# Kernel optimization log

Hardware: AMD Instinct MI355X
Metric: run time of the kernel (lower is better)

The kernel has to match this reference:

```python
import jax, jax.numpy as jnp
import numpy as np

NUM_HEADS = 16


def setup_inputs() -> dict:
    key = jax.random.key(0)
    k1, k2, k3 = jax.random.split(key, 3)
    B, N, C = 2, 2048, 1024
    x = jax.random.normal(k1, (B, N, C), dtype=jnp.float32)
    w_qkv = jax.random.normal(k2, (3 * C, C), dtype=jnp.float32) * (C ** -0.5)
    w_proj = jax.random.normal(k3, (C, C), dtype=jnp.float32) * (C ** -0.5)
    b_proj = jnp.zeros((C,), dtype=jnp.float32)
    return {"x": x, "w_qkv": w_qkv, "w_proj": w_proj, "b_proj": b_proj}


def reference(x, w_qkv, w_proj, b_proj):
    B, N, C = x.shape
    H = NUM_HEADS
    D = C // H
    scale = 1.0 / jnp.sqrt(jnp.asarray(D, x.dtype))
    qkv = (x @ w_qkv.T).reshape(B, N, 3, H, D)
    qkv = jnp.transpose(qkv, (2, 0, 3, 1, 4))  # [3,B,H,N,D]
    q, k, v = qkv[0], qkv[1], qkv[2]
    # scaled dot-product attention with explicit score matrix [B,H,N,N]
    attn = jnp.einsum('bhnd,bhmd->bhnm', q, k) * scale
    attn = jax.nn.softmax(attn, axis=-1)
    out = jnp.einsum('bhnm,bhmd->bhnd', attn, v)
    out = jnp.transpose(out, (0, 2, 1, 3)).reshape(B, N, C)
    # output projection
    return out @ w_proj.T + b_proj
```

## Files before the change

kernel.cpp:

```cpp
#include <hip/hip_runtime.h>

typedef unsigned short u16;
typedef __attribute__((ext_vector_type(8))) short bf16x8;
typedef __attribute__((ext_vector_type(4))) float f32x4;
typedef __attribute__((ext_vector_type(16))) float f32x16;
typedef __attribute__((ext_vector_type(4))) unsigned u32x4;

#define B_ 2
#define N_ 2048
#define C_ 1024
#define H_ 16
#define D_ 64
#define M_ (B_ * N_)

#define QSCALE 0.18033688011114336f

#define EXP2R(x) __builtin_amdgcn_exp2f(x)

__device__ __forceinline__ u16 f2bf(float f) {
    union { float f; unsigned u; } x; x.f = f;
    return (u16)((x.u + 0x8000u) >> 16);
}
__device__ __forceinline__ unsigned pack2bf(float a, float b) {
    union { float f; unsigned u; } x, y; x.f = a; y.f = b;
    return __builtin_amdgcn_perm(y.u + 0x8000u, x.u + 0x8000u, 0x07060302);
}
__device__ __forceinline__ unsigned cvtpk2bf(float a, float b) {
    unsigned r;
    asm("v_cvt_pk_bf16_f32 %0, %1, %2" : "=v"(r) : "v"(a), "v"(b));
    return r;
}

__device__ __forceinline__ void async_copy16(const void* gsrc, void* ldst) {
    __builtin_amdgcn_global_load_lds(
        (__attribute__((address_space(1))) void*)gsrc,
        (__attribute__((address_space(3))) void*)ldst,
        16, 0, 0);
}

__global__ void cast3_kernel(const float* __restrict__ x, const float* __restrict__ wq,
                             const float* __restrict__ wp, u16* __restrict__ xo,
                             u16* __restrict__ wqo, u16* __restrict__ wpo) {
    int b = blockIdx.x;
    const float* s; u16* d;
    if (b < 4096)      { s = x;  d = xo;  }
    else if (b < 7168) { s = wq; d = wqo; b -= 4096; }
    else               { s = wp; d = wpo; b -= 7168; }
    int i = (b * 256 + threadIdx.x) * 4;
    const float4 v = *(const float4*)(s + i);
    uint2 o;
    o.x = pack2bf(v.x, v.y);
    o.y = pack2bf(v.z, v.w);
    *(uint2*)(d + i) = o;
}

__global__ __launch_bounds__(512, 2) void gemm_qkv8(
    const u16* __restrict__ A, const u16* __restrict__ Bm,
    u16* __restrict__ qo, u16* __restrict__ ko, u16* __restrict__ vt) {
    __shared__ u16 L[2][4][8192];
    const int tid = threadIdx.x, lane = tid & 63, w = tid >> 6;
    const int wm = w >> 2, wn = w & 3;
    const int q16 = lane >> 4, l15 = lane & 15, l7 = lane & 7;
    const int lr3 = lane >> 3, lc7 = lane & 7;
    const int sbid = (blockIdx.x & 7) * 24 + (blockIdx.x >> 3);
    const int bx = sbid % 12, by = sbid / 12;
    const int m0 = by * 256, n0 = bx * 256;
    const int cswz8 = (lc7 ^ lr3) * 8;

    auto stageHT = [&](int t, int isB, int h) {
        if (t > 15) return;
        const u16* src = isB ? Bm : A;
        int base_row = (isB ? n0 : m0) + h * 128;
#pragma unroll
        for (int i = 0; i < 2; ++i) {
            int c = w * 2 + i;
            async_copy16(src + (size_t)(base_row + c * 8 + lr3) * 1024 + t * 64 + cswz8,
                         (char*)L + ((t & 1) * 4 + isB * 2 + h) * 16384 + c * 1024);
        }
    };

    stageHT(0, 0, 0); stageHT(0, 1, 0); stageHT(0, 1, 1); stageHT(0, 0, 1);
    stageHT(1, 0, 0); stageHT(1, 1, 0); stageHT(1, 1, 1);
    asm volatile("s_waitcnt vmcnt(6)" ::: "memory");
    __builtin_amdgcn_s_barrier();

    f32x4 acc[8][4] = {};
    const int aRow = l15 * 64;
    const int colsw0 = (q16 ^ l7) * 8, colsw1 = ((4 + q16) ^ l7) * 8;
    const u16* LA[2] = { &L[0][wm][0], &L[1][wm][0] };
    const u16* LB[2] = { &L[0][2 + (wn >> 1)][0], &L[1][2 + (wn >> 1)][0] };
    const int bOff = (wn & 1) * 4096;

    bf16x8 Af[4][2], Bf0[2][2], Bf1[2][2];

    auto readA = [&](int P, int mh) {
#pragma unroll
        for (int i = 0; i < 4; ++i) {
            Af[i][0] = *(const bf16x8*)(LA[P] + (mh * 64 + i * 16) * 64 + aRow + colsw0);
            Af[i][1] = *(const bf16x8*)(LA[P] + (mh * 64 + i * 16) * 64 + aRow + colsw1);
        }
    };
    auto readB = [&](int P, int nh, bf16x8 (*Bf)[2]) {
#pragma unroll
        for (int j = 0; j < 2; ++j) {
            Bf[j][0] = *(const bf16x8*)(LB[P] + bOff + (nh * 32 + j * 16) * 64 + aRow + colsw0);
            Bf[j][1] = *(const bf16x8*)(LB[P] + bOff + (nh * 32 + j * 16) * 64 + aRow + colsw1);
        }
    };
    auto mfma16 = [&](int mh, int nh, bf16x8 (*Bf)[2]) {
        __builtin_amdgcn_s_setprio(1);
#pragma unroll
        for (int i = 0; i < 4; ++i)
#pragma unroll
            for (int j = 0; j < 2; ++j)
#pragma unroll
                for (int ks = 0; ks < 2; ++ks)
                    acc[mh * 4 + i][nh * 2 + j] = __builtin_amdgcn_mfma_f32_16x16x32_bf16(
                        Af[i][ks], Bf[j][ks], acc[mh * 4 + i][nh * 2 + j], 0, 0, 0);
        __builtin_amdgcn_s_setprio(0);
    };

    for (int it = 0; it < 8; ++it) {
        const int T = 2 * it;
        readA(0, 0); readB(0, 0, Bf0); stageHT(T + 1, 0, 1);
        __builtin_amdgcn_s_barrier();
        mfma16(0, 0, Bf0);
        __builtin_amdgcn_s_barrier();
        readB(0, 1, Bf1);
        __builtin_amdgcn_s_barrier();
        mfma16(0, 1, Bf1);
        __builtin_amdgcn_s_barrier();
        readA(0, 1); stageHT(T + 2, 1, 0);
        __builtin_amdgcn_s_barrier();
        mfma16(1, 1, Bf1);
        __builtin_amdgcn_s_barrier();
        stageHT(T + 2, 1, 1); stageHT(T + 2, 0, 0);
        __builtin_amdgcn_s_barrier();
        mfma16(1, 0, Bf0);
        if (it < 7) { asm volatile("s_waitcnt vmcnt(6)" ::: "memory"); }
        else        { asm volatile("s_waitcnt vmcnt(0)" ::: "memory"); }
        __builtin_amdgcn_s_barrier();
        readA(1, 0); readB(1, 0, Bf0); stageHT(T + 2, 0, 1);
        __builtin_amdgcn_s_barrier();
        mfma16(0, 0, Bf0);
        __builtin_amdgcn_s_barrier();
        readB(1, 1, Bf1);
        __builtin_amdgcn_s_barrier();
        mfma16(0, 1, Bf1);
        __builtin_amdgcn_s_barrier();
        readA(1, 1); stageHT(T + 3, 1, 0);
        __builtin_amdgcn_s_barrier();
        mfma16(1, 1, Bf1);
        __builtin_amdgcn_s_barrier();
        stageHT(T + 3, 1, 1); stageHT(T + 3, 0, 0);
        __builtin_amdgcn_s_barrier();
        mfma16(1, 0, Bf0);
        if (it < 7) { asm volatile("s_waitcnt vmcnt(6)" ::: "memory"); }
        __builtin_amdgcn_s_barrier();
    }

#pragma unroll
    for (int fm = 0; fm < 8; ++fm) {
#pragma unroll
        for (int fn = 0; fn < 4; ++fn) {
            int n_g = n0 + wn * 64 + fn * 16 + l15;
            int which = n_g >> 10;
            int h = (n_g >> 6) & 15;
            int d = n_g & 63;
            int m_base = m0 + wm * 128 + fm * 16 + q16 * 4;
            int b = m_base >> 11;
            int nn0 = m_base & 2047;
            if (which == 2) {
                uint2 pk;
                pk.x = pack2bf(acc[fm][fn][0], acc[fm][fn][1]);
                pk.y = pack2bf(acc[fm][fn][2], acc[fm][fn][3]);
                *(uint2*)(vt + ((size_t)((b * H_ + h) * D_ + d) << 11) + nn0) = pk;
            } else {
                size_t base = ((size_t)((b * H_ + h) * N_ + nn0) << 6) + d;
#pragma unroll
                for (int r = 0; r < 4; ++r) {
                    float v = acc[fm][fn][r];
                    if (which == 0) qo[base + (size_t)r * D_] = f2bf(v * QSCALE);
                    else            ko[base + (size_t)r * D_] = f2bf(v);
                }
            }
        }
    }
}

__global__ __launch_bounds__(256, 2) void gemm_out(
    const u16* __restrict__ A, const u16* __restrict__ Bm,
    const float* __restrict__ bias, float* __restrict__ out) {
    __shared__ u16 As[128 * 64];
    __shared__ u16 Bs[64 * 64];
    const int K = C_, Ncols = C_, ntiles_n = 16;
    const int tid = threadIdx.x, lane = tid & 63, w = tid >> 6;
    const int cpx = gridDim.x >> 3;
    const int sbid = (blockIdx.x & 7) * cpx + (blockIdx.x >> 3);
    const int bx = sbid % ntiles_n, by = sbid / ntiles_n;
    const int m0 = by * 128, n0 = bx * 64;
    const int wm = w >> 1, wn = w & 1;
    const int q16 = lane >> 4, l15 = lane & 15;
    const int r0 = lane >> 3, c0 = (lane & 7) * 8;
    f32x4 acc[4][2] = {};

    for (int k0 = 0; k0 < K; k0 += 64) {
#pragma unroll
        for (int i = 0; i < 4; ++i) {
            int blk = w * 4 + i;
            int r = blk * 8 + r0;
            async_copy16(A + (size_t)(m0 + r) * K + k0 + c0, (char*)As + blk * 1024);
        }
#pragma unroll
        for (int i = 0; i < 2; ++i) {
            int blk = w * 2 + i;
            int r = blk * 8 + r0;
            async_copy16(Bm + (size_t)(n0 + r) * K + k0 + c0, (char*)Bs + blk * 1024);
        }
        __builtin_amdgcn_s_waitcnt(0);
        __syncthreads();
#pragma unroll
        for (int ks = 0; ks < 2; ++ks) {
            bf16x8 af[4], bf[2];
#pragma unroll
            for (int i = 0; i < 4; ++i)
                af[i] = *(const bf16x8*)&As[(wm * 64 + i * 16 + l15) * 64 + ks * 32 + q16 * 8];
#pragma unroll
            for (int i = 0; i < 2; ++i)
                bf[i] = *(const bf16x8*)&Bs[(wn * 32 + i * 16 + l15) * 64 + ks * 32 + q16 * 8];
#pragma unroll
            for (int mi = 0; mi < 4; ++mi)
#pragma unroll
                for (int ni = 0; ni < 2; ++ni)
                    acc[mi][ni] = __builtin_amdgcn_mfma_f32_16x16x32_bf16(af[mi], bf[ni], acc[mi][ni], 0, 0, 0);
        }
        __syncthreads();
    }

#pragma unroll
    for (int mi = 0; mi < 4; ++mi) {
#pragma unroll
        for (int ni = 0; ni < 2; ++ni) {
            int n_g = n0 + wn * 32 + ni * 16 + l15;
#pragma unroll
            for (int r = 0; r < 4; ++r) {
                int m_g = m0 + wm * 64 + mi * 16 + q16 * 4 + r;
                out[(size_t)m_g * Ncols + n_g] = acc[mi][ni][r] + bias[n_g];
            }
        }
    }
}

__global__ __launch_bounds__(512, 1) void attn_kernel(
    const u16* __restrict__ Q, const u16* __restrict__ K,
    const u16* __restrict__ VT, u16* __restrict__ O) {
    __shared__ u16 Ks[2][2][64 * 64];
    __shared__ u16 Vs[2][2][64 * 64];
    const int tid = threadIdx.x, lane = tid & 63, w = tid >> 6;
    const int l31 = lane & 31, hi = lane >> 5, l7 = l31 & 7;
    const int bid = blockIdx.x;
    const int bh = (bid & 7) * 4 + (bid >> 6);
    const int q0 = ((bid >> 3) & 7) * 256;
    const size_t head = (size_t)bh * N_ * D_;
    const int lr3 = lane >> 3, lc7 = lane & 7;

    auto stage = [&](int kt, int buf) {
        int key0 = kt * 128;
        int row = w * 8 + lr3;
#pragma unroll
        for (int s = 0; s < 2; ++s) {
            async_copy16(K + head + (size_t)(key0 + s * 64 + row) * D_ + (lc7 ^ lr3) * 8,
                         (char*)Ks[buf][s] + w * 1024);
            async_copy16(VT + head + (size_t)row * N_ + key0 + s * 64 + (lc7 ^ lr3) * 8,
                         (char*)Vs[buf][s] + w * 1024);
        }
    };

    bf16x8 qf[4];
#pragma unroll
    for (int ds = 0; ds < 4; ++ds)
        qf[ds] = *(const bf16x8*)(Q + head + (size_t)(q0 + w * 32 + l31) * D_ + ds * 16 + hi * 8);
    stage(0, 0);
    __builtin_amdgcn_s_waitcnt(0);
    __syncthreads();

    f32x16 o_acc[2] = {};
    float rs = 0.f;

    for (int kt = 0; kt < 16; ++kt) {
        int buf = kt & 1;
        stage((kt + 1) & 15, buf ^ 1);

#pragma unroll
        for (int s = 0; s < 2; ++s) {
#pragma unroll
            for (int kb2 = 0; kb2 < 2; ++kb2) {
                f32x16 st = {};
                __builtin_amdgcn_s_setprio(1);
#pragma unroll
                for (int ds = 0; ds < 4; ++ds) {
                    bf16x8 kf = *(const bf16x8*)&Ks[buf][s][(kb2 * 32 + l31) * 64 + ((ds * 2 + hi) ^ l7) * 8];
                    st = __builtin_amdgcn_mfma_f32_32x32x16_bf16(kf, qf[ds], st, 0, 0, 0);
                }
                __builtin_amdgcn_s_setprio(0);

                float p[16];
#pragma unroll
                for (int i = 0; i < 16; ++i) p[i] = EXP2R(st[i]);
#pragma unroll
                for (int i = 0; i < 16; ++i) rs += p[i];

                unsigned a0 = cvtpk2bf(p[0], p[1]),   b0 = cvtpk2bf(p[4], p[5]);
                unsigned a1 = cvtpk2bf(p[2], p[3]),   b1 = cvtpk2bf(p[6], p[7]);
                unsigned a2 = cvtpk2bf(p[8], p[9]),   b2 = cvtpk2bf(p[12], p[13]);
                unsigned a3 = cvtpk2bf(p[10], p[11]), b3 = cvtpk2bf(p[14], p[15]);
                asm("v_permlane32_swap_b32 %0, %1" : "+v"(a0), "+v"(b0));
                asm("v_permlane32_swap_b32 %0, %1" : "+v"(a1), "+v"(b1));
                asm("v_permlane32_swap_b32 %0, %1" : "+v"(a2), "+v"(b2));
                asm("v_permlane32_swap_b32 %0, %1" : "+v"(a3), "+v"(b3));
                union { u32x4 u; bf16x8 v; } af0, af1;
                af0.u = (u32x4){a0, a1, b0, b1};
                af1.u = (u32x4){a2, a3, b2, b3};

                __builtin_amdgcn_s_setprio(1);
#pragma unroll
                for (int db = 0; db < 2; ++db) {
                    bf16x8 vf0 = *(const bf16x8*)&Vs[buf][s][(db * 32 + l31) * 64 + ((kb2 * 4 + hi) ^ l7) * 8];
                    o_acc[db] = __builtin_amdgcn_mfma_f32_32x32x16_bf16(af0.v, vf0, o_acc[db], 0, 0, 0);
                    bf16x8 vf1 = *(const bf16x8*)&Vs[buf][s][(db * 32 + l31) * 64 + ((kb2 * 4 + 2 + hi) ^ l7) * 8];
                    o_acc[db] = __builtin_amdgcn_mfma_f32_32x32x16_bf16(af1.v, vf1, o_acc[db], 0, 0, 0);
                }
                __builtin_amdgcn_s_setprio(0);
            }
        }

        __builtin_amdgcn_s_waitcnt(0);
        __syncthreads();
    }

    rs += __shfl_xor(rs, 32);
    float rsi = 1.0f / rs;

    const int b = bh >> 4, h = bh & 15;
#pragma unroll
    for (int reg = 0; reg < 16; ++reg) {
        int qrow = (reg & 3) + 8 * (reg >> 2) + 4 * hi;
        float inv = __shfl(rsi, qrow);
        int qg = q0 + w * 32 + qrow;
#pragma unroll
        for (int db = 0; db < 2; ++db) {
            int d = db * 32 + l31;
            O[((size_t)(b * N_ + qg) << 10) + h * 64 + d] = f2bf(o_acc[db][reg] * inv);
        }
    }
}

extern "C" void kernel_launch(void* const* d_in, const int* in_sizes, int n_in,
                              void* d_out, int out_size, void* d_ws, size_t ws_size,
                              hipStream_t stream) {
    const float* x      = (const float*)d_in[0];
    const float* w_qkv  = (const float*)d_in[1];
    const float* w_proj = (const float*)d_in[2];
    const float* b_proj = (const float*)d_in[3];
    float* out = (float*)d_out;

    char* ws = (char*)d_ws;
    const size_t MB = 1024 * 1024;
    u16* x_bf     = (u16*)(ws + 0 * MB);
    u16* wqkv_bf  = (u16*)(ws + 8 * MB);
    u16* wproj_bf = (u16*)(ws + 14 * MB);
    u16* q_bf     = (u16*)(ws + 16 * MB);
    u16* k_bf     = (u16*)(ws + 24 * MB);
    u16* vt_bf    = (u16*)(ws + 32 * MB);
    u16* ao_bf    = (u16*)(ws + 40 * MB);

    cast3_kernel<<<8192, 256, 0, stream>>>(x, w_qkv, w_proj, x_bf, wqkv_bf, wproj_bf);

    gemm_qkv8<<<192, 512, 0, stream>>>(x_bf, wqkv_bf, q_bf, k_bf, vt_bf);

    attn_kernel<<<256, 512, 0, stream>>>(q_bf, k_bf, vt_bf, ao_bf);

    gemm_out<<<512, 256, 0, stream>>>(ao_bf, wproj_bf, b_proj, out);
}
```

Baseline: 175.4 us.

## Fuse cast, QKV GEMM, attention and output GEMM into persistent mega-kernel

```diff
diff --git a/kernel.cpp b/kernel.cpp
--- a/kernel.cpp
+++ b/kernel.cpp
@@ -36,6 +36,342 @@
         (__attribute__((address_space(1))) void*)gsrc,
         (__attribute__((address_space(3))) void*)ldst,
         16, 0, 0);
+}
+
+__device__ __forceinline__ void gbar(unsigned* bar) {
+    __syncthreads();
+    __threadfence();
+    if (threadIdx.x == 0) {
+        unsigned g = __hip_atomic_load(bar + 1, __ATOMIC_ACQUIRE, __HIP_MEMORY_SCOPE_AGENT);
+        unsigned old = __hip_atomic_fetch_add(bar, 1, __ATOMIC_ACQ_REL, __HIP_MEMORY_SCOPE_AGENT);
+        if (old == 255) {
+            __hip_atomic_store(bar, 0, __ATOMIC_RELAXED, __HIP_MEMORY_SCOPE_AGENT);
+            __hip_atomic_fetch_add(bar + 1, 1, __ATOMIC_ACQ_REL, __HIP_MEMORY_SCOPE_AGENT);
+        } else {
+            while (__hip_atomic_load(bar + 1, __ATOMIC_ACQUIRE, __HIP_MEMORY_SCOPE_AGENT) == g)
+                __builtin_amdgcn_s_sleep(2);
+        }
+    }
+    __syncthreads();
+}
+
+__global__ __launch_bounds__(512, 1) void mega_kernel(
+    const float* __restrict__ x, const float* __restrict__ wq,
+    const float* __restrict__ wp, const float* __restrict__ bias,
+    u16* __restrict__ x_bf, u16* __restrict__ wqkv_bf, u16* __restrict__ wproj_bf,
+    u16* __restrict__ q_bf, u16* __restrict__ k_bf, u16* __restrict__ vt_bf,
+    u16* __restrict__ ao_bf, float* __restrict__ out, unsigned* bar) {
+    __shared__ __align__(16) u16 SL[65536];
+    const int tid = threadIdx.x, bid = blockIdx.x;
+    const int lane = tid & 63, w = tid >> 6;
+
+    for (int i4 = bid * 512 + tid; i4 < 2097152; i4 += 256 * 512) {
+        const float* s; u16* d; int j = i4;
+        if (j < 1048576)      { s = x;  d = x_bf; }
+        else if (j < 1835008) { s = wq; d = wqkv_bf; j -= 1048576; }
+        else                  { s = wp; d = wproj_bf; j -= 1835008; }
+        const float4 v = *(const float4*)(s + (size_t)j * 4);
+        uint2 o;
+        o.x = pack2bf(v.x, v.y);
+        o.y = pack2bf(v.z, v.w);
+        *(uint2*)(d + (size_t)j * 4) = o;
+    }
+    gbar(bar);
+
+    if (bid < 192) {
+        u16* L = SL;
+        const int wm = w >> 2, wn = w & 3;
+        const int q16 = lane >> 4, l15 = lane & 15, l7 = lane & 7;
+        const int lr3 = lane >> 3, lc7 = lane & 7;
+        const int sbid = (bid & 7) * 24 + (bid >> 3);
+        const int bx = sbid % 12, by = sbid / 12;
+        const int m0 = by * 256, n0 = bx * 256;
+        const int cswz8 = (lc7 ^ lr3) * 8;
+
+        auto stageHT = [&](int t, int isB, int h) {
+            if (t > 15) return;
+            const u16* src = isB ? wqkv_bf : x_bf;
+            int base_row = (isB ? n0 : m0) + h * 128;
+#pragma unroll
+            for (int i = 0; i < 2; ++i) {
+                int c = w * 2 + i;
+                async_copy16(src + (size_t)(base_row + c * 8 + lr3) * 1024 + t * 64 + cswz8,
+                             (char*)L + ((t & 1) * 4 + isB * 2 + h) * 16384 + c * 1024);
+            }
+        };
+
+        stageHT(0, 0, 0); stageHT(0, 1, 0); stageHT(0, 1, 1); stageHT(0, 0, 1);
+        stageHT(1, 0, 0); stageHT(1, 1, 0); stageHT(1, 1, 1);
+        asm volatile("s_waitcnt vmcnt(6)" ::: "memory");
+        __builtin_amdgcn_s_barrier();
+
+        f32x4 acc[8][4] = {};
+        const int aRow = l15 * 64;
+        const int colsw0 = (q16 ^ l7) * 8, colsw1 = ((4 + q16) ^ l7) * 8;
+        const u16* LA[2] = { L + (0 * 4 + wm) * 8192, L + (1 * 4 + wm) * 8192 };
+        const u16* LB[2] = { L + (0 * 4 + 2 + (wn >> 1)) * 8192, L + (1 * 4 + 2 + (wn >> 1)) * 8192 };
+        const int bOff = (wn & 1) * 4096;
+
+        bf16x8 Af[4][2], Bf0[2][2], Bf1[2][2];
+
+        auto readA = [&](int P, int mh) {
+#pragma unroll
+            for (int i = 0; i < 4; ++i) {
+                Af[i][0] = *(const bf16x8*)(LA[P] + (mh * 64 + i * 16) * 64 + aRow + colsw0);
+                Af[i][1] = *(const bf16x8*)(LA[P] + (mh * 64 + i * 16) * 64 + aRow + colsw1);
+            }
+        };
+        auto readB = [&](int P, int nh, bf16x8 (*Bf)[2]) {
+#pragma unroll
+            for (int j = 0; j < 2; ++j) {
+                Bf[j][0] = *(const bf16x8*)(LB[P] + bOff + (nh * 32 + j * 16) * 64 + aRow + colsw0);
+                Bf[j][1] = *(const bf16x8*)(LB[P] + bOff + (nh * 32 + j * 16) * 64 + aRow + colsw1);
+            }
+        };
+        auto mfma16 = [&](int mh, int nh, bf16x8 (*Bf)[2]) {
+            __builtin_amdgcn_s_setprio(1);
+#pragma unroll
+            for (int i = 0; i < 4; ++i)
+#pragma unroll
+                for (int j = 0; j < 2; ++j)
+#pragma unroll
+                    for (int ks = 0; ks < 2; ++ks)
+                        acc[mh * 4 + i][nh * 2 + j] = __builtin_amdgcn_mfma_f32_16x16x32_bf16(
+                            Af[i][ks], Bf[j][ks], acc[mh * 4 + i][nh * 2 + j], 0, 0, 0);
+            __builtin_amdgcn_s_setprio(0);
+        };
+
+        for (int it = 0; it < 8; ++it) {
+            const int T = 2 * it;
+            readA(0, 0); readB(0, 0, Bf0); stageHT(T + 1, 0, 1);
+            __builtin_amdgcn_s_barrier();
+            mfma16(0, 0, Bf0);
+            __builtin_amdgcn_s_barrier();
+            readB(0, 1, Bf1);
+            __builtin_amdgcn_s_barrier();
+            mfma16(0, 1, Bf1);
+            __builtin_amdgcn_s_barrier();
+            readA(0, 1); stageHT(T + 2, 1, 0);
+            __builtin_amdgcn_s_barrier();
+            mfma16(1, 1, Bf1);
+            __builtin_amdgcn_s_barrier();
+            stageHT(T + 2, 1, 1); stageHT(T + 2, 0, 0);
+            __builtin_amdgcn_s_barrier();
+            mfma16(1, 0, Bf0);
+            if (it < 7) { asm volatile("s_waitcnt vmcnt(6)" ::: "memory"); }
+            else        { asm volatile("s_waitcnt vmcnt(0)" ::: "memory"); }
+            __builtin_amdgcn_s_barrier();
+            readA(1, 0); readB(1, 0, Bf0); stageHT(T + 2, 0, 1);
+            __builtin_amdgcn_s_barrier();
+            mfma16(0, 0, Bf0);
+            __builtin_amdgcn_s_barrier();
+            readB(1, 1, Bf1);
+            __builtin_amdgcn_s_barrier();
+            mfma16(0, 1, Bf1);
+            __builtin_amdgcn_s_barrier();
+            readA(1, 1); stageHT(T + 3, 1, 0);
+            __builtin_amdgcn_s_barrier();
+            mfma16(1, 1, Bf1);
+            __builtin_amdgcn_s_barrier();
+            stageHT(T + 3, 1, 1); stageHT(T + 3, 0, 0);
+            __builtin_amdgcn_s_barrier();
+            mfma16(1, 0, Bf0);
+            if (it < 7) { asm volatile("s_waitcnt vmcnt(6)" ::: "memory"); }
+            __builtin_amdgcn_s_barrier();
+        }
+
+#pragma unroll
+        for (int fm = 0; fm < 8; ++fm) {
+#pragma unroll
+            for (int fn = 0; fn < 4; ++fn) {
+                int n_g = n0 + wn * 64 + fn * 16 + l15;
+                int which = n_g >> 10;
+                int h = (n_g >> 6) & 15;
+                int d = n_g & 63;
+                int m_base = m0 + wm * 128 + fm * 16 + q16 * 4;
+                int b = m_base >> 11;
+                int nn0 = m_base & 2047;
+                if (which == 2) {
+                    uint2 pk;
+                    pk.x = pack2bf(acc[fm][fn][0], acc[fm][fn][1]);
+                    pk.y = pack2bf(acc[fm][fn][2], acc[fm][fn][3]);
+                    *(uint2*)(vt_bf + ((size_t)((b * H_ + h) * D_ + d) << 11) + nn0) = pk;
+                } else {
+                    size_t base = ((size_t)((b * H_ + h) * N_ + nn0) << 6) + d;
+#pragma unroll
+                    for (int r = 0; r < 4; ++r) {
+                        float v = acc[fm][fn][r];
+                        if (which == 0) q_bf[base + (size_t)r * D_] = f2bf(v * QSCALE);
+                        else            k_bf[base + (size_t)r * D_] = f2bf(v);
+                    }
+                }
+            }
+        }
+    }
+    gbar(bar);
+
+    {
+        u16* KsB = SL;
+        u16* VsB = SL + 16384;
+        const int l31 = lane & 31, hi = lane >> 5, l7 = l31 & 7;
+        const int bh = (bid & 7) * 4 + (bid >> 6);
+        const int q0 = ((bid >> 3) & 7) * 256;
+        const size_t head = (size_t)bh * N_ * D_;
+        const int lr3 = lane >> 3, lc7 = lane & 7;
+
+        auto stage = [&](int kt, int buf) {
+            int key0 = kt * 128;
+            int row = w * 8 + lr3;
+#pragma unroll
+            for (int s = 0; s < 2; ++s) {
+                async_copy16(k_bf + head + (size_t)(key0 + s * 64 + row) * D_ + (lc7 ^ lr3) * 8,
+                             (char*)(KsB + (buf * 2 + s) * 4096) + w * 1024);
+                async_copy16(vt_bf + head + (size_t)row * N_ + key0 + s * 64 + (lc7 ^ lr3) * 8,
+                             (char*)(VsB + (buf * 2 + s) * 4096) + w * 1024);
+            }
+        };
+
+        bf16x8 qf[4];
+#pragma unroll
+        for (int ds = 0; ds < 4; ++ds)
+            qf[ds] = *(const bf16x8*)(q_bf + head + (size_t)(q0 + w * 32 + l31) * D_ + ds * 16 + hi * 8);
+        stage(0, 0);
+        __builtin_amdgcn_s_waitcnt(0);
+        __syncthreads();
+
+        f32x16 o_acc[2] = {};
+        float rs = 0.f;
+
+        for (int kt = 0; kt < 16; ++kt) {
+            int buf = kt & 1;
+            stage((kt + 1) & 15, buf ^ 1);
+
+#pragma unroll
+            for (int s = 0; s < 2; ++s) {
+                const u16* Kp = KsB + (buf * 2 + s) * 4096;
+                const u16* Vp = VsB + (buf * 2 + s) * 4096;
+#pragma unroll
+                for (int kb2 = 0; kb2 < 2; ++kb2) {
+                    f32x16 st = {};
+                    __builtin_amdgcn_s_setprio(1);
+#pragma unroll
+                    for (int ds = 0; ds < 4; ++ds) {
+                        bf16x8 kf = *(const bf16x8*)(Kp + (kb2 * 32 + l31) * 64 + ((ds * 2 + hi) ^ l7) * 8);
+                        st = __builtin_amdgcn_mfma_f32_32x32x16_bf16(kf, qf[ds], st, 0, 0, 0);
+                    }
+                    __builtin_amdgcn_s_setprio(0);
+
+                    float p[16];
+#pragma unroll
+                    for (int i = 0; i < 16; ++i) p[i] = EXP2R(st[i]);
+#pragma unroll
+                    for (int i = 0; i < 16; ++i) rs += p[i];
+
+                    unsigned a0 = cvtpk2bf(p[0], p[1]),   b0 = cvtpk2bf(p[4], p[5]);
+                    unsigned a1 = cvtpk2bf(p[2], p[3]),   b1 = cvtpk2bf(p[6], p[7]);
+                    unsigned a2 = cvtpk2bf(p[8], p[9]),   b2 = cvtpk2bf(p[12], p[13]);
+                    unsigned a3 = cvtpk2bf(p[10], p[11]), b3 = cvtpk2bf(p[14], p[15]);
+                    asm("v_permlane32_swap_b32 %0, %1" : "+v"(a0), "+v"(b0));
+                    asm("v_permlane32_swap_b32 %0, %1" : "+v"(a1), "+v"(b1));
+                    asm("v_permlane32_swap_b32 %0, %1" : "+v"(a2), "+v"(b2));
+                    asm("v_permlane32_swap_b32 %0, %1" : "+v"(a3), "+v"(b3));
+                    union { u32x4 u; bf16x8 v; } af0, af1;
+                    af0.u = (u32x4){a0, a1, b0, b1};
+                    af1.u = (u32x4){a2, a3, b2, b3};
+
+                    __builtin_amdgcn_s_setprio(1);
+#pragma unroll
+                    for (int db = 0; db < 2; ++db) {
+                        bf16x8 vf0 = *(const bf16x8*)(Vp + (db * 32 + l31) * 64 + ((kb2 * 4 + hi) ^ l7) * 8);
+                        o_acc[db] = __builtin_amdgcn_mfma_f32_32x32x16_bf16(af0.v, vf0, o_acc[db], 0, 0, 0);
+                        bf16x8 vf1 = *(const bf16x8*)(Vp + (db * 32 + l31) * 64 + ((kb2 * 4 + 2 + hi) ^ l7) * 8);
+                        o_acc[db] = __builtin_amdgcn_mfma_f32_32x32x16_bf16(af1.v, vf1, o_acc[db], 0, 0, 0);
+                    }
+                    __builtin_amdgcn_s_setprio(0);
+                }
+            }
+
+            __builtin_amdgcn_s_waitcnt(0);
+            __syncthreads();
+        }
+
+        rs += __shfl_xor(rs, 32);
+        float rsi = 1.0f / rs;
+        const int b = bh >> 4, h = bh & 15;
+#pragma unroll
+        for (int reg = 0; reg < 16; ++reg) {
+            int qrow = (reg & 3) + 8 * (reg >> 2) + 4 * hi;
+            float inv = __shfl(rsi, qrow);
+            int qg = q0 + w * 32 + qrow;
+#pragma unroll
+            for (int db = 0; db < 2; ++db) {
+                int d = db * 32 + l31;
+                ao_bf[((size_t)(b * N_ + qg) << 10) + h * 64 + d] = f2bf(o_acc[db][reg] * inv);
+            }
+        }
+    }
+    gbar(bar);
+
+    {
+        const int grp = w >> 2, wv = w & 2 ? (w & 3) : (w & 3);
+        const int wv3 = w & 3;
+        u16* As = SL + grp * 12288;
+        u16* Bs = SL + grp * 12288 + 8192;
+        const int v = bid * 2 + grp;
+        const int sbid = (v & 7) * 64 + (v >> 3);
+        const int bx = sbid & 15, by = sbid >> 4;
+        const int m0 = by * 128, n0 = bx * 64;
+        const int wm = wv3 >> 1, wn = wv3 & 1;
+        const int q16 = lane >> 4, l15 = lane & 15;
+        const int r0 = lane >> 3, c0 = (lane & 7) * 8;
+        f32x4 acc[4][2] = {};
+
+        for (int k0 = 0; k0 < C_; k0 += 64) {
+#pragma unroll
+            for (int i = 0; i < 4; ++i) {
+                int blk = wv3 * 4 + i;
+                int r = blk * 8 + r0;
+                async_copy16(ao_bf + (size_t)(m0 + r) * C_ + k0 + c0, (char*)As + blk * 1024);
+            }
+#pragma unroll
+            for (int i = 0; i < 2; ++i) {
+                int blk = wv3 * 2 + i;
+                int r = blk * 8 + r0;
+                async_copy16(wproj_bf + (size_t)(n0 + r) * C_ + k0 + c0, (char*)Bs + blk * 1024);
+            }
+            __builtin_amdgcn_s_waitcnt(0);
+            __syncthreads();
+#pragma unroll
+            for (int ks = 0; ks < 2; ++ks) {
+                bf16x8 af[4], bf[2];
+#pragma unroll
+                for (int i = 0; i < 4; ++i)
+                    af[i] = *(const bf16x8*)(As + (wm * 64 + i * 16 + l15) * 64 + ks * 32 + q16 * 8);
+#pragma unroll
+                for (int i = 0; i < 2; ++i)
+                    bf[i] = *(const bf16x8*)(Bs + (wn * 32 + i * 16 + l15) * 64 + ks * 32 + q16 * 8);
+#pragma unroll
+                for (int mi = 0; mi < 4; ++mi)
+#pragma unroll
+                    for (int ni = 0; ni < 2; ++ni)
+                        acc[mi][ni] = __builtin_amdgcn_mfma_f32_16x16x32_bf16(af[mi], bf[ni], acc[mi][ni], 0, 0, 0);
+            }
+            __syncthreads();
+        }
+
+#pragma unroll
+        for (int mi = 0; mi < 4; ++mi) {
+#pragma unroll
+            for (int ni = 0; ni < 2; ++ni) {
+                int n_g = n0 + wn * 32 + ni * 16 + l15;
+#pragma unroll
+                for (int r = 0; r < 4; ++r) {
+                    int m_g = m0 + wm * 64 + mi * 16 + q16 * 4 + r;
+                    out[(size_t)m_g * C_ + n_g] = acc[mi][ni][r] + bias[n_g];
+                }
+            }
+        }
+    }
 }
 
 __global__ void cast3_kernel(const float* __restrict__ x, const float* __restrict__ wq,
@@ -54,132 +390,70 @@
     *(uint2*)(d + i) = o;
 }
 
-__global__ __launch_bounds__(512, 2) void gemm_qkv8(
+__global__ __launch_bounds__(256, 3) void gemm_qkv(
     const u16* __restrict__ A, const u16* __restrict__ Bm,
     u16* __restrict__ qo, u16* __restrict__ ko, u16* __restrict__ vt) {
-    __shared__ u16 L[2][4][8192];
+    __shared__ u16 As[128 * 64];
+    __shared__ u16 Bs[128 * 64];
+    const int K = C_, ntiles_n = 24;
     const int tid = threadIdx.x, lane = tid & 63, w = tid >> 6;
-    const int wm = w >> 2, wn = w & 3;
-    const int q16 = lane >> 4, l15 = lane & 15, l7 = lane & 7;
-    const int lr3 = lane >> 3, lc7 = lane & 7;
-    const int sbid = (blockIdx.x & 7) * 24 + (blockIdx.x >> 3);
-    const int bx = sbid % 12, by = sbid / 12;
-    const int m0 = by * 256, n0 = bx * 256;
-    const int cswz8 = (lc7 ^ lr3) * 8;
-
-    auto stageHT = [&](int t, int isB, int h) {
-        if (t > 15) return;
-        const u16* src = isB ? Bm : A;
-        int base_row = (isB ? n0 : m0) + h * 128;
-#pragma unroll
-        for (int i = 0; i < 2; ++i) {
-            int c = w * 2 + i;
-            async_copy16(src + (size_t)(base_row + c * 8 + lr3) * 1024 + t * 64 + cswz8,
-                         (char*)L + ((t & 1) * 4 + isB * 2 + h) * 16384 + c * 1024);
-        }
-    };
-
-    stageHT(0, 0, 0); stageHT(0, 1, 0); stageHT(0, 1, 1); stageHT(0, 0, 1);
-    stageHT(1, 0, 0); stageHT(1, 1, 0); stageHT(1, 1, 1);
-    asm volatile("s_waitcnt vmcnt(6)" ::: "memory");
-    __builtin_amdgcn_s_barrier();
-
-    f32x4 acc[8][4] = {};
-    const int aRow = l15 * 64;
-    const int colsw0 = (q16 ^ l7) * 8, colsw1 = ((4 + q16) ^ l7) * 8;
-    const u16* LA[2] = { &L[0][wm][0], &L[1][wm][0] };
-    const u16* LB[2] = { &L[0][2 + (wn >> 1)][0], &L[1][2 + (wn >> 1)][0] };
-    const int bOff = (wn & 1) * 4096;
-
-    bf16x8 Af[4][2], Bf0[2][2], Bf1[2][2];
-
-    auto readA = [&](int P, int mh) {
+    const int cpx = gridDim.x >> 3;
+    const int sbid = (blockIdx.x & 7) * cpx + (blockIdx.x >> 3);
+    const int bx = sbid % ntiles_n, by = sbid / ntiles_n;
+    const int m0 = by * 128, n0 = bx * 128;
+    const int wm = w >> 1, wn = w & 1;
+    const int q16 = lane >> 4, l15 = lane & 15;
+    const int r0 = lane >> 3, c0 = (lane & 7) * 8;
+    f32x4 acc[4][4] = {};
+
+    for (int k0 = 0; k0 < K; k0 += 64) {
 #pragma unroll
         for (int i = 0; i < 4; ++i) {
-            Af[i][0] = *(const bf16x8*)(LA[P] + (mh * 64 + i * 16) * 64 + aRow + colsw0);
-            Af[i][1] = *(const bf16x8*)(LA[P] + (mh * 64 + i * 16) * 64 + aRow + colsw1);
-        }
-    };
-    auto readB = [&](int P, int nh, bf16x8 (*Bf)[2]) {
-#pragma unroll
-        for (int j = 0; j < 2; ++j) {
-            Bf[j][0] = *(const bf16x8*)(LB[P] + bOff + (nh * 32 + j * 16) * 64 + aRow + colsw0);
-            Bf[j][1] = *(const bf16x8*)(LB[P] + bOff + (nh * 32 + j * 16) * 64 + aRow + colsw1);
-        }
-    };
-    auto mfma16 = [&](int mh, int nh, bf16x8 (*Bf)[2]) {
-        __builtin_amdgcn_s_setprio(1);
-#pragma unroll
-        for (int i = 0; i < 4; ++i)
-#pragma unroll
-            for (int j = 0; j < 2; ++j)
-#pragma unroll
-                for (int ks = 0; ks < 2; ++ks)
-                    acc[mh * 4 + i][nh * 2 + j] = __builtin_amdgcn_mfma_f32_16x16x32_bf16(
-                        Af[i][ks], Bf[j][ks], acc[mh * 4 + i][nh * 2 + j], 0, 0, 0);
-        __builtin_amdgcn_s_setprio(0);
-    };
-
-    for (int it = 0; it < 8; ++it) {
-        const int T = 2 * it;
-        readA(0, 0); readB(0, 0, Bf0); stageHT(T + 1, 0, 1);
-        __builtin_amdgcn_s_barrier();
-        mfma16(0, 0, Bf0);
-        __builtin_amdgcn_s_barrier();
-        readB(0, 1, Bf1);
-        __builtin_amdgcn_s_barrier();
-        mfma16(0, 1, Bf1);
-        __builtin_amdgcn_s_barrier();
-        readA(0, 1); stageHT(T + 2, 1, 0);
-        __builtin_amdgcn_s_barrier();
-        mfma16(1, 1, Bf1);
-        __builtin_amdgcn_s_barrier();
-        stageHT(T + 2, 1, 1); stageHT(T + 2, 0, 0);
-        __builtin_amdgcn_s_barrier();
-        mfma16(1, 0, Bf0);
-        if (it < 7) { asm volatile("s_waitcnt vmcnt(6)" ::: "memory"); }
-        else        { asm volatile("s_waitcnt vmcnt(0)" ::: "memory"); }
-        __builtin_amdgcn_s_barrier();
-        readA(1, 0); readB(1, 0, Bf0); stageHT(T + 2, 0, 1);
-        __builtin_amdgcn_s_barrier();
-        mfma16(0, 0, Bf0);
-        __builtin_amdgcn_s_barrier();
-        readB(1, 1, Bf1);
-        __builtin_amdgcn_s_barrier();
-        mfma16(0, 1, Bf1);
-        __builtin_amdgcn_s_barrier();
-        readA(1, 1); stageHT(T + 3, 1, 0);
-        __builtin_amdgcn_s_barrier();
-        mfma16(1, 1, Bf1);
-        __builtin_amdgcn_s_barrier();
-        stageHT(T + 3, 1, 1); stageHT(T + 3, 0, 0);
-        __builtin_amdgcn_s_barrier();
-        mfma16(1, 0, Bf0);
-        if (it < 7) { asm volatile("s_waitcnt vmcnt(6)" ::: "memory"); }
-        __builtin_amdgcn_s_barrier();
-    }
-
-#pragma unroll
-    for (int fm = 0; fm < 8; ++fm) {
-#pragma unroll
-        for (int fn = 0; fn < 4; ++fn) {
-            int n_g = n0 + wn * 64 + fn * 16 + l15;
+            int blk = w * 4 + i;
+            int r = blk * 8 + r0;
+            async_copy16(A + (size_t)(m0 + r) * K + k0 + c0, (char*)As + blk * 1024);
+            async_copy16(Bm + (size_t)(n0 + r) * K + k0 + c0, (char*)Bs + blk * 1024);
+        }
+        __builtin_amdgcn_s_waitcnt(0);
+        __syncthreads();
+#pragma unroll
+        for (int ks = 0; ks < 2; ++ks) {
+            bf16x8 af[4], bf[4];
+#pragma unroll
+            for (int i = 0; i < 4; ++i) {
+                af[i] = *(const bf16x8*)&As[(wm * 64 + i * 16 + l15) * 64 + ks * 32 + q16 * 8];
+                bf[i] = *(const bf16x8*)&Bs[(wn * 64 + i * 16 + l15) * 64 + ks * 32 + q16 * 8];
+            }
+#pragma unroll
+            for (int mi = 0; mi < 4; ++mi)
+#pragma unroll
+                for (int ni = 0; ni < 4; ++ni)
+                    acc[mi][ni] = __builtin_amdgcn_mfma_f32_16x16x32_bf16(af[mi], bf[ni], acc[mi][ni], 0, 0, 0);
+        }
+        __syncthreads();
+    }
+
+#pragma unroll
+    for (int mi = 0; mi < 4; ++mi) {
+#pragma unroll
+        for (int ni = 0; ni < 4; ++ni) {
+            int n_g = n0 + wn * 64 + ni * 16 + l15;
             int which = n_g >> 10;
             int h = (n_g >> 6) & 15;
             int d = n_g & 63;
-            int m_base = m0 + wm * 128 + fm * 16 + q16 * 4;
+            int m_base = m0 + wm * 64 + mi * 16 + q16 * 4;
             int b = m_base >> 11;
             int nn0 = m_base & 2047;
             if (which == 2) {
                 uint2 pk;
-                pk.x = pack2bf(acc[fm][fn][0], acc[fm][fn][1]);
-                pk.y = pack2bf(acc[fm][fn][2], acc[fm][fn][3]);
+                pk.x = pack2bf(acc[mi][ni][0], acc[mi][ni][1]);
+                pk.y = pack2bf(acc[mi][ni][2], acc[mi][ni][3]);
                 *(uint2*)(vt + ((size_t)((b * H_ + h) * D_ + d) << 11) + nn0) = pk;
             } else {
                 size_t base = ((size_t)((b * H_ + h) * N_ + nn0) << 6) + d;
 #pragma unroll
                 for (int r = 0; r < 4; ++r) {
-                    float v = acc[fm][fn][r];
+                    float v = acc[mi][ni][r];
                     if (which == 0) qo[base + (size_t)r * D_] = f2bf(v * QSCALE);
                     else            ko[base + (size_t)r * D_] = f2bf(v);
                 }
@@ -188,7 +462,7 @@
     }
 }
 
-__global__ __launch_bounds__(256, 2) void gemm_out(
+__global__ __launch_bounds__(256, 2) void gemm_out_k(
     const u16* __restrict__ A, const u16* __restrict__ Bm,
     const float* __restrict__ bias, float* __restrict__ out) {
     __shared__ u16 As[128 * 64];
@@ -374,11 +648,16 @@
     u16* vt_bf    = (u16*)(ws + 32 * MB);
     u16* ao_bf    = (u16*)(ws + 40 * MB);
 
-    cast3_kernel<<<8192, 256, 0, stream>>>(x, w_qkv, w_proj, x_bf, wqkv_bf, wproj_bf);
-
-    gemm_qkv8<<<192, 512, 0, stream>>>(x_bf, wqkv_bf, q_bf, k_bf, vt_bf);
-
-    attn_kernel<<<256, 512, 0, stream>>>(q_bf, k_bf, vt_bf, ao_bf);
-
-    gemm_out<<<512, 256, 0, stream>>>(ao_bf, wproj_bf, b_proj, out);
-}
+    if (ws_size >= 48 * MB + 64) {
+        unsigned* bar = (unsigned*)(ws + 48 * MB);
+        hipMemsetAsync(bar, 0, 64, stream);
+        mega_kernel<<<256, 512, 0, stream>>>(x, w_qkv, w_proj, b_proj,
+                                             x_bf, wqkv_bf, wproj_bf,
+                                             q_bf, k_bf, vt_bf, ao_bf, out, bar);
+    } else {
+        cast3_kernel<<<8192, 256, 0, stream>>>(x, w_qkv, w_proj, x_bf, wqkv_bf, wproj_bf);
+        gemm_qkv<<<768, 256, 0, stream>>>(x_bf, wqkv_bf, q_bf, k_bf, vt_bf);
+        attn_kernel<<<256, 512, 0, stream>>>(q_bf, k_bf, vt_bf, ao_bf);
+        gemm_out_k<<<512, 256, 0, stream>>>(ao_bf, wproj_bf, b_proj, out);
+    }
+}
```

Measured after the change: 450.3 us. 2.57x slower.
